# Performance work log

Hardware: AMD Instinct MI355X
Metric: run time of the kernel (lower is better)

The kernel has to match this reference:

```python
import jax, jax.numpy as jnp
import numpy as np

N_NODES = 100_000
N_EDGES = 1_600_000  # random edges; self-loops appended (add_self_edges_networkx)
IN_FEATS = 64
N_HIDDEN = 64
N_CLASSES = 40


def setup_inputs() -> dict:
    key = jax.random.key(0)
    ks = jax.random.split(key, 10)
    features = jax.random.normal(ks[0], (N_NODES, IN_FEATS), jnp.float32)
    self_loops = jnp.arange(N_NODES, dtype=jnp.int32)
    src = jnp.concatenate([jax.random.randint(ks[1], (N_EDGES,), 0, N_NODES, jnp.int32), self_loops])
    dst = jnp.concatenate([jax.random.randint(ks[2], (N_EDGES,), 0, N_NODES, jnp.int32), self_loops])
    labels = jax.random.randint(ks[3], (N_NODES,), 0, N_CLASSES, jnp.int32)
    mask = jnp.ones((N_NODES,), bool)
    s = 0.05
    W0 = jax.random.normal(ks[4], (IN_FEATS, N_HIDDEN), jnp.float32) * s
    b0 = jnp.zeros((N_HIDDEN,), jnp.float32)
    W1 = jax.random.normal(ks[5], (N_HIDDEN, N_HIDDEN), jnp.float32) * s
    b1 = jnp.zeros((N_HIDDEN,), jnp.float32)
    W2 = jax.random.normal(ks[6], (N_HIDDEN, N_CLASSES), jnp.float32) * s
    b2 = jnp.zeros((N_CLASSES,), jnp.float32)
    return {"features": features, "W0": W0, "b0": b0, "W1": W1, "b1": b1,
            "W2": W2, "b2": b2, "src": src, "dst": dst,
            "labels": labels, "mask": mask}


def reference(features, W0, b0, W1, b1, W2, b2, src, dst, labels, mask):
    # gcn_msg: pass src 'h'; gcn_reduce: sum over incoming messages;
    # NodeApplyModule: linear (+ activation on non-final layers).
    def gcn_layer(h, W, b, act):
        agg = jax.ops.segment_sum(h[src], dst, num_segments=N_NODES)  # gather -> sum reduce
        h = agg @ W + b
        return jax.nn.relu(h) if act else h

    h = gcn_layer(features, W0, b0, act=True)
    h = gcn_layer(h, W1, b1, act=True)
    rep = gcn_layer(h, W2, b2, act=False)  # [N, n_classes]

    # loss: fn_reduce=log_softmax over dim=0 (as written in the source), nll sum / count
    logp = jax.nn.log_softmax(rep, axis=0)
    picked = jnp.take_along_axis(logp, labels[:, None].astype(jnp.int32), axis=1)[:, 0]
    maskf = mask.astype(jnp.float32)
    loss = -jnp.sum(picked * maskf) / jnp.sum(maskf)
    return rep, loss
```

## Files before the change

### kernel.cpp

```cpp
#include <hip/hip_runtime.h>
#include <hip/hip_bf16.h>
#include <hip/hip_fp16.h>

#define NCLS 40

typedef __attribute__((ext_vector_type(8))) _Float16 half8;
typedef __attribute__((ext_vector_type(2))) _Float16 half2h;
union H2U { half2h h; unsigned u; };

#define EPB 16384
#define MAXB1 128
#define MAXNB 104

__global__ void bucket_hist(const int* __restrict__ dst, int E, int nb,
                            int* __restrict__ blockHist) {
    __shared__ int cnt[4][MAXNB];
    int t = threadIdx.x;
    for (int i = t; i < 4 * MAXNB; i += 256) cnt[i / MAXNB][i % MAXNB] = 0;
    __syncthreads();
    int bk = t & 3;
    int base = blockIdx.x * EPB;
    int end = min(base + EPB, E);
    for (int i = base + t; i < end; i += 256) atomicAdd(&cnt[bk][dst[i] >> 10], 1);
    __syncthreads();
    for (int i = t; i < nb; i += 256)
        blockHist[blockIdx.x * nb + i] = cnt[0][i] + cnt[1][i] + cnt[2][i] + cnt[3][i];
}

__global__ void bucket_scan(const int* __restrict__ blockHist, int nB1, int nb,
                            int* __restrict__ blockBase, int* __restrict__ bucketOffs,
                            int* __restrict__ offs, int N, int E, int* __restrict__ red32) {
    __shared__ int h[MAXB1 * MAXNB];
    __shared__ int btot[MAXNB];
    __shared__ int boffs[MAXNB + 1];
    int t = threadIdx.x;
    if (t < 128) red32[t] = 0;
    int total = nB1 * nb;
    for (int i = t; i < total; i += 128) h[i] = blockHist[i];
    __syncthreads();
    for (int b = t; b < nb; b += 128) {
        int run = 0;
        for (int i = 0; i < nB1; ++i) { int v = h[i * nb + b]; h[i * nb + b] = run; run += v; }
        btot[b] = run;
    }
    __syncthreads();
    if (t == 0) {
        int run = 0;
        for (int b = 0; b < nb; ++b) { boffs[b] = run; run += btot[b]; }
        boffs[nb] = run;
    }
    __syncthreads();
    for (int b = t; b < nb; b += 128) {
        int bo = boffs[b];
        for (int i = 0; i < nB1; ++i) h[i * nb + b] += bo;
    }
    __syncthreads();
    for (int i = t; i < total; i += 128) blockBase[i] = h[i];
    for (int b = t; b <= nb; b += 128) bucketOffs[b] = boffs[b];
    if (t == 0) offs[N] = E;
}

__global__ void bucket_place(const int* __restrict__ src, const int* __restrict__ dst, int E,
                             int nb, const int* __restrict__ blockBase,
                             unsigned* __restrict__ tmp) {
    __shared__ int cur[MAXNB];
    int t = threadIdx.x;
    for (int i = t; i < nb; i += 256) cur[i] = blockBase[blockIdx.x * nb + i];
    __syncthreads();
    int base = blockIdx.x * EPB;
    int end = min(base + EPB, E);
    for (int i = base + t; i < end; i += 256) {
        int d = dst[i];
        int s = src[i];
        unsigned pack = ((unsigned)(d & 1023) << 17) | (unsigned)s;
        int pos = atomicAdd(&cur[d >> 10], 1);
        tmp[pos] = pack;
    }
}

__global__ __launch_bounds__(512) void bucket_finalize(const unsigned* __restrict__ tmp,
                                                       const int* __restrict__ bucketOffs,
                                                       int N, int* __restrict__ offs,
                                                       int* __restrict__ esrc) {
    __shared__ int cnt[1024];
    __shared__ int wsum[8];
    int b = blockIdx.x;
    int t = threadIdx.x;
    int bstart = bucketOffs[b], bend = bucketOffs[b + 1];
    cnt[t] = 0;
    cnt[t + 512] = 0;
    __syncthreads();
    for (int i = bstart + t; i < bend; i += 512) atomicAdd(&cnt[tmp[i] >> 17], 1);
    __syncthreads();
    int c0 = cnt[2 * t], c1 = cnt[2 * t + 1];
    int s = c0 + c1;
    int lane = t & 63, w = t >> 6;
    int ssc = s;
    for (int off = 1; off < 64; off <<= 1) {
        int v = __shfl_up(ssc, off, 64);
        if (lane >= off) ssc += v;
    }
    if (lane == 63) wsum[w] = ssc;
    __syncthreads();
    int wo = 0;
#pragma unroll
    for (int k = 0; k < 8; ++k)
        if (k < w) wo += wsum[k];
    int excl = (ssc - s) + wo + bstart;
    __syncthreads();
    int node0 = (b << 10) + 2 * t;
    if (node0 < N) offs[node0] = excl;
    if (node0 + 1 < N) offs[node0 + 1] = excl + c0;
    cnt[2 * t] = excl;
    cnt[2 * t + 1] = excl + c0;
    __syncthreads();
    for (int i = bstart + t; i < bend; i += 512) {
        unsigned p = tmp[i];
        int pos = atomicAdd(&cnt[p >> 17], 1);
        esrc[pos] = (int)(p & 0x1FFFFu);
    }
}

__global__ __launch_bounds__(256) void gemm_fdot(const void* __restrict__ X, int xHalf,
                                                 const float* __restrict__ W,
                                                 const float* __restrict__ bias,
                                                 void* __restrict__ out, int outHalf,
                                                 int N, int FO) {
    int lane = threadIdx.x & 63;
    int waveId = (blockIdx.x * blockDim.x + threadIdx.x) >> 6;
    int nWaves = (gridDim.x * blockDim.x) >> 6;
    int cl = lane < FO ? lane : 0;
    int p = lane & 31;

    H2U wh[32];
#pragma unroll
    for (int j = 0; j < 32; ++j)
        wh[j].h = half2h{(_Float16)W[(2 * j) * FO + cl], (_Float16)W[(2 * j + 1) * FO + cl]};
    float gb = 0.f;
    if (bias != nullptr && lane < FO) gb = bias[lane];

    const unsigned* Xh = (const unsigned*)X;
    const float2* Xf = (const float2*)X;
    float* outF = (float*)out;
    _Float16* outH = (_Float16*)out;

    auto loadX = [&](int row) -> H2U {
        H2U r; r.u = 0;
        if (row < N) {
            if (xHalf) r.u = Xh[(size_t)row * 32 + p];
            else {
                float2 f = Xf[(size_t)row * 32 + p];
                r.h = half2h{(_Float16)f.x, (_Float16)f.y};
            }
        }
        return r;
    };

    int row = waveId;
    H2U xp = loadX(row);
    for (; row < N; row += nWaves) {
        H2U nxt = loadX(row + nWaves);
        float y0 = gb, y1 = 0.f;
#pragma unroll
        for (int j2 = 0; j2 < 32; j2 += 2) {
            H2U r0, r1;
            r0.u = __builtin_amdgcn_readlane(xp.u, j2);
            r1.u = __builtin_amdgcn_readlane(xp.u, j2 + 1);
            y0 = __builtin_amdgcn_fdot2(r0.h, wh[j2].h, y0, false);
            y1 = __builtin_amdgcn_fdot2(r1.h, wh[j2 + 1].h, y1, false);
        }
        float y = y0 + y1;
        if (lane < FO) {
            if (outHalf) outH[(size_t)row * FO + lane] = (_Float16)y;
            else         outF[(size_t)row * FO + lane] = y;
        }
        xp = nxt;
    }
}

__global__ void agg64h_kernel(const _Float16* __restrict__ t, const int* __restrict__ offs,
                              const int* __restrict__ esrc, const float* __restrict__ bias,
                              _Float16* __restrict__ out, int N, int doRelu) {
    int gid = blockIdx.x * blockDim.x + threadIdx.x;
    int node = gid >> 6;
    if (node >= N) return;
    int lane = threadIdx.x & 63;
    int sub = lane >> 3;
    int c8 = lane & 7;
    int beg = offs[node], end = offs[node + 1];
    half8 acc0 = {};
    half8 acc1 = {};
    int j = beg + sub;
    for (; j + 8 < end; j += 16) {
        int s0 = esrc[j];
        int s1 = esrc[j + 8];
        half8 v0 = *(const half8*)(t + (size_t)s0 * 64 + c8 * 8);
        half8 v1 = *(const half8*)(t + (size_t)s1 * 64 + c8 * 8);
        acc0 += v0;
        acc1 += v1;
    }
    if (j < end) {
        int s0 = esrc[j];
        acc0 += *(const half8*)(t + (size_t)s0 * 64 + c8 * 8);
    }
    half8 acc = acc0 + acc1;
    float a[8];
#pragma unroll
    for (int k = 0; k < 8; ++k) a[k] = (float)acc[k];
#pragma unroll
    for (int k = 0; k < 8; ++k) {
        a[k] += __shfl_down(a[k], 32, 64);
        a[k] += __shfl_down(a[k], 16, 64);
        a[k] += __shfl_down(a[k], 8, 64);
    }
    if (sub == 0) {
        half8 hv;
#pragma unroll
        for (int k = 0; k < 8; ++k) {
            float v = a[k];
            if (bias != nullptr) v += bias[c8 * 8 + k];
            if (doRelu) v = fmaxf(v, 0.f);
            hv[k] = (_Float16)v;
        }
        *(half8*)(out + (size_t)node * 64 + c8 * 8) = hv;
    }
}

__global__ void loss_pass(const float* __restrict__ rep, const int* __restrict__ labels, int N,
                          double* __restrict__ colSum, double* __restrict__ pickedSum,
                          int* __restrict__ cnt) {
    const int G = 8;
    const int ROWS = 512;
    int t = threadIdx.x;
    int c = t % NCLS;
    int g = t / NCLS;
    int base = blockIdx.x * ROWS;
    int lim = min(base + ROWS, N);
    double sumLoc = 0.0, pickLoc = 0.0;
    int cntLoc = 0;
    for (int r = base + g; r < lim; r += G) {
        float v = rep[(size_t)r * NCLS + c];
        sumLoc += exp((double)v);
        if (labels[r] == c) { pickLoc += (double)v; cntLoc++; }
    }
    __shared__ double colP[G][NCLS];
    __shared__ int cntP[G][NCLS];
    __shared__ double waveP[5];
    colP[g][c] = sumLoc;
    cntP[g][c] = cntLoc;
    __syncthreads();
    if (g == 0) {
        double tot = 0.0;
        int ctot = 0;
        for (int gg = 0; gg < G; ++gg) { tot += colP[gg][c]; ctot += cntP[gg][c]; }
        atomicAdd(&colSum[c], tot);
        if (ctot) atomicAdd(&cnt[c], ctot);
    }
    double wv = pickLoc;
    for (int off = 32; off; off >>= 1) wv += __shfl_down(wv, off, 64);
    if ((t & 63) == 0) waveP[t >> 6] = wv;
    __syncthreads();
    if (t == 0) {
        double s = 0.0;
        for (int i = 0; i < 5; ++i) s += waveP[i];
        atomicAdd(pickedSum, s);
    }
}

__global__ void finalize_kernel(const double* __restrict__ colSum, const int* __restrict__ cnt,
                                const double* __restrict__ pickedSum, int N,
                                float* __restrict__ lossOut) {
    int t = threadIdx.x;
    double term = 0.0;
    if (t < NCLS) term = (double)cnt[t] * log(colSum[t]);
    for (int off = 32; off; off >>= 1) term += __shfl_down(term, off, 64);
    if (t == 0) lossOut[0] = (float)((term - pickedSum[0]) / (double)N);
}

extern "C" void kernel_launch(void* const* d_in, const int* in_sizes, int n_in,
                              void* d_out, int out_size, void* d_ws, size_t ws_size,
                              hipStream_t stream) {
    const float* features = (const float*)d_in[0];
    const float* W0 = (const float*)d_in[1];
    const float* b0 = (const float*)d_in[2];
    const float* W1 = (const float*)d_in[3];
    const float* b1 = (const float*)d_in[4];
    const float* W2 = (const float*)d_in[5];
    const float* b2 = (const float*)d_in[6];
    const int* src = (const int*)d_in[7];
    const int* dst = (const int*)d_in[8];
    const int* labels = (const int*)d_in[9];

    const int N = in_sizes[0] / 64;
    const int E = in_sizes[7];
    const int NC = in_sizes[6];

    char* ws = (char*)d_ws;
    size_t off = 0;
    auto alloc = [&](size_t bytes) -> void* {
        void* p = ws + off;
        off = (off + bytes + 255) & ~(size_t)255;
        return p;
    };
    int* offs      = (int*)alloc((size_t)(N + 1) * 4);
    int* esrc      = (int*)alloc((size_t)E * 4);
    _Float16* bufA = (_Float16*)alloc((size_t)N * 64 * 2);
    _Float16* bufB = (_Float16*)alloc((size_t)N * 64 * 2);
    int* blockHist = (int*)alloc((size_t)MAXB1 * MAXNB * 4);
    int* blockBase = (int*)alloc((size_t)MAXB1 * MAXNB * 4);
    int* bucketOffs= (int*)alloc((size_t)(MAXNB + 1) * 4);
    char* red      = (char*)alloc(512);
    double* colSum    = (double*)red;
    double* pickedSum = (double*)(red + 320);
    int* cntRed       = (int*)(red + 328);

    unsigned* tmp = (unsigned*)bufA;

    float* rep = (float*)d_out;
    float* lossOut = rep + (size_t)N * NC;

    const int nb  = (N + 1023) >> 10;
    const int nB1 = (E + EPB - 1) / EPB;

    bucket_hist<<<nB1, 256, 0, stream>>>(dst, E, nb, blockHist);
    bucket_scan<<<1, 128, 0, stream>>>(blockHist, nB1, nb, blockBase, bucketOffs, offs, N, E,
                                       (int*)red);
    bucket_place<<<nB1, 256, 0, stream>>>(src, dst, E, nb, blockBase, tmp);
    bucket_finalize<<<nb, 512, 0, stream>>>(tmp, bucketOffs, N, offs, esrc);

    const int nodeWaveBlocks = (N * 64 + 255) / 256;

    gemm_fdot<<<2048, 256, 0, stream>>>(features, 0, W0, nullptr, bufA, 1, N, 64);
    agg64h_kernel<<<nodeWaveBlocks, 256, 0, stream>>>(bufA, offs, esrc, b0, bufB, N, 1);
    gemm_fdot<<<2048, 256, 0, stream>>>(bufB, 1, W1, nullptr, bufA, 1, N, 64);
    agg64h_kernel<<<nodeWaveBlocks, 256, 0, stream>>>(bufA, offs, esrc, b1, bufB, N, 1);
    agg64h_kernel<<<nodeWaveBlocks, 256, 0, stream>>>(bufB, offs, esrc, nullptr, bufA, N, 0);
    gemm_fdot<<<2048, 256, 0, stream>>>(bufA, 1, W2, b2, rep, 0, N, NC);

    loss_pass<<<(N + 511) / 512, 320, 0, stream>>>(rep, labels, N, colSum, pickedSum, cntRed);
    finalize_kernel<<<1, 64, 0, stream>>>(colSum, cntRed, pickedSum, N, lossOut);
}
```

Measured before the change: 433.9 us.

## Transform before aggregating in last GCN layer; accumulate in fp32

The last layer now applies W2 first, producing a 40-wide fp16 table, and then aggregates that table with a new 40-column gather kernel that adds the bias and writes fp32 rep directly. This moves the last layer's transform ahead of aggregation, so the edge gather reads narrower rows and the final matmul has no separate fp32 pass. The 64-wide aggregation kernel now accumulates in fp32 rather than fp16, which costs more conversion ALU work but improves precision. In the 40-wide kernel only 5 of the 8 lane groups do useful work, and its 80-byte rows do not line up with 128-byte lines.

```diff
diff --git a/kernel.cpp b/kernel.cpp
--- a/kernel.cpp
+++ b/kernel.cpp
@@ -180,7 +180,7 @@
 
 __global__ void agg64h_kernel(const _Float16* __restrict__ t, const int* __restrict__ offs,
                               const int* __restrict__ esrc, const float* __restrict__ bias,
-                              _Float16* __restrict__ out, int N, int doRelu) {
+                              _Float16* __restrict__ out, int N) {
     int gid = blockIdx.x * blockDim.x + threadIdx.x;
     int node = gid >> 6;
     if (node >= N) return;
@@ -188,25 +188,24 @@
     int sub = lane >> 3;
     int c8 = lane & 7;
     int beg = offs[node], end = offs[node + 1];
-    half8 acc0 = {};
-    half8 acc1 = {};
+    float a[8];
+#pragma unroll
+    for (int k = 0; k < 8; ++k) a[k] = 0.f;
     int j = beg + sub;
     for (; j + 8 < end; j += 16) {
         int s0 = esrc[j];
         int s1 = esrc[j + 8];
         half8 v0 = *(const half8*)(t + (size_t)s0 * 64 + c8 * 8);
         half8 v1 = *(const half8*)(t + (size_t)s1 * 64 + c8 * 8);
-        acc0 += v0;
-        acc1 += v1;
+#pragma unroll
+        for (int k = 0; k < 8; ++k) a[k] += (float)v0[k] + (float)v1[k];
     }
     if (j < end) {
         int s0 = esrc[j];
-        acc0 += *(const half8*)(t + (size_t)s0 * 64 + c8 * 8);
-    }
-    half8 acc = acc0 + acc1;
-    float a[8];
-#pragma unroll
-    for (int k = 0; k < 8; ++k) a[k] = (float)acc[k];
+        half8 v0 = *(const half8*)(t + (size_t)s0 * 64 + c8 * 8);
+#pragma unroll
+        for (int k = 0; k < 8; ++k) a[k] += (float)v0[k];
+    }
 #pragma unroll
     for (int k = 0; k < 8; ++k) {
         a[k] += __shfl_down(a[k], 32, 64);
@@ -217,12 +216,58 @@
         half8 hv;
 #pragma unroll
         for (int k = 0; k < 8; ++k) {
-            float v = a[k];
-            if (bias != nullptr) v += bias[c8 * 8 + k];
-            if (doRelu) v = fmaxf(v, 0.f);
+            float v = fmaxf(a[k] + bias[c8 * 8 + k], 0.f);
             hv[k] = (_Float16)v;
         }
         *(half8*)(out + (size_t)node * 64 + c8 * 8) = hv;
+    }
+}
+
+__global__ void agg40h_kernel(const _Float16* __restrict__ u, const int* __restrict__ offs,
+                              const int* __restrict__ esrc, const float* __restrict__ bias,
+                              float* __restrict__ rep, int N) {
+    int gid = blockIdx.x * blockDim.x + threadIdx.x;
+    int node = gid >> 6;
+    if (node >= N) return;
+    int lane = threadIdx.x & 63;
+    int sub = lane >> 3;
+    int c8 = lane & 7;
+    int beg = offs[node], end = offs[node + 1];
+    float a[8];
+#pragma unroll
+    for (int k = 0; k < 8; ++k) a[k] = 0.f;
+    if (c8 < 5) {
+        int j = beg + sub;
+        for (; j + 8 < end; j += 16) {
+            int s0 = esrc[j];
+            int s1 = esrc[j + 8];
+            half8 v0 = *(const half8*)(u + (size_t)s0 * 40 + c8 * 8);
+            half8 v1 = *(const half8*)(u + (size_t)s1 * 40 + c8 * 8);
+#pragma unroll
+            for (int k = 0; k < 8; ++k) a[k] += (float)v0[k] + (float)v1[k];
+        }
+        if (j < end) {
+            int s0 = esrc[j];
+            half8 v0 = *(const half8*)(u + (size_t)s0 * 40 + c8 * 8);
+#pragma unroll
+            for (int k = 0; k < 8; ++k) a[k] += (float)v0[k];
+        }
+    }
+#pragma unroll
+    for (int k = 0; k < 8; ++k) {
+        a[k] += __shfl_down(a[k], 32, 64);
+        a[k] += __shfl_down(a[k], 16, 64);
+        a[k] += __shfl_down(a[k], 8, 64);
+    }
+    if (sub == 0 && c8 < 5) {
+        float* po = rep + (size_t)node * NCLS + c8 * 8;
+        float4 r0, r1;
+        r0.x = a[0] + bias[c8 * 8 + 0]; r0.y = a[1] + bias[c8 * 8 + 1];
+        r0.z = a[2] + bias[c8 * 8 + 2]; r0.w = a[3] + bias[c8 * 8 + 3];
+        r1.x = a[4] + bias[c8 * 8 + 4]; r1.y = a[5] + bias[c8 * 8 + 5];
+        r1.z = a[6] + bias[c8 * 8 + 6]; r1.w = a[7] + bias[c8 * 8 + 7];
+        *(float4*)(po) = r0;
+        *(float4*)(po + 4) = r1;
     }
 }
 
@@ -331,11 +376,11 @@
     const int nodeWaveBlocks = (N * 64 + 255) / 256;
 
     gemm_fdot<<<2048, 256, 0, stream>>>(features, 0, W0, nullptr, bufA, 1, N, 64);
-    agg64h_kernel<<<nodeWaveBlocks, 256, 0, stream>>>(bufA, offs, esrc, b0, bufB, N, 1);
+    agg64h_kernel<<<nodeWaveBlocks, 256, 0, stream>>>(bufA, offs, esrc, b0, bufB, N);
     gemm_fdot<<<2048, 256, 0, stream>>>(bufB, 1, W1, nullptr, bufA, 1, N, 64);
-    agg64h_kernel<<<nodeWaveBlocks, 256, 0, stream>>>(bufA, offs, esrc, b1, bufB, N, 1);
-    agg64h_kernel<<<nodeWaveBlocks, 256, 0, stream>>>(bufB, offs, esrc, nullptr, bufA, N, 0);
-    gemm_fdot<<<2048, 256, 0, stream>>>(bufA, 1, W2, b2, rep, 0, N, NC);
+    agg64h_kernel<<<nodeWaveBlocks, 256, 0, stream>>>(bufA, offs, esrc, b1, bufB, N);
+    gemm_fdot<<<2048, 256, 0, stream>>>(bufB, 1, W2, nullptr, bufA, 1, N, NC);
+    agg40h_kernel<<<nodeWaveBlocks, 256, 0, stream>>>(bufA, offs, esrc, b2, rep, N);
 
     loss_pass<<<(N + 511) / 512, 320, 0, stream>>>(rep, labels, N, colSum, pickedSum, cntRed);
     finalize_kernel<<<1, 64, 0, stream>>>(colSum, cntRed, pickedSum, N, lossOut);
```

New measurement: 400.6 us. 7.7% less time.
